# Performance work log

Hardware: AMD Instinct MI355X
Metric: run time of the kernel (lower is better)

## Reference

```python
import jax, jax.numpy as jnp
import numpy as np

# irreps structure: 256x0e + 128x1e + 64x2e (same for all three layers)
MULS = [256, 128, 64]
DIMS = [1, 3, 5]  # 2l+1 for l=0,1,2


def _split(x):
    """Split flat feature [N, 960] into per-irrep blocks [N, mul, 2l+1]."""
    blocks, o = [], 0
    for m, d in zip(MULS, DIMS):
        blocks.append(x[:, o:o + m * d].reshape(-1, m, d))
        o += m * d
    return blocks


def _merge(blocks):
    n = blocks[0].shape[0]
    return jnp.concatenate([b.reshape(n, -1) for b in blocks], axis=1)


def _irrep_linear(blocks, ws):
    # o3.Linear between identical irreps: per-l matmul over the multiplicity
    # axis, path_normalization='element' (single path) -> scale 1/sqrt(mul_in).
    return [jnp.einsum('nui,uw->nwi', b, w) / np.sqrt(b.shape[1])
            for b, w in zip(blocks, ws)]


def _norm_act(blocks):
    # e3nn NormActivation(gelu), normalize=True: x * gelu(||x||) / ||x||
    out = []
    for b in blocks:
        n = jnp.sqrt(jnp.sum(b * b, axis=-1, keepdims=True))  # [N, mul, 1]
        safe_n = jnp.where(n > 0, n, 1.0)
        out.append(b * (jax.nn.gelu(n, approximate=False) / safe_n))
    return out


def setup_inputs() -> dict:
    key = jax.random.key(0)
    ks = jax.random.split(key, 7)
    N = 65536
    D = sum(m * d for m, d in zip(MULS, DIMS))  # 960
    inp = {'x': jax.random.normal(ks[0], (N, D), dtype=jnp.float32)}
    names = ['W0_0', 'W0_1', 'W0_2', 'W1_0', 'W1_1', 'W1_2']
    shapes = [(256, 256), (128, 128), (64, 64)] * 2
    for k, name, s in zip(ks[1:], names, shapes):
        inp[name] = jax.random.normal(k, s, dtype=jnp.float32)
    return inp


def reference(x, W0_0, W0_1, W0_2, W1_0, W1_1, W1_2):
    blocks = _split(x)
    blocks = _irrep_linear(blocks, [W0_0, W0_1, W0_2])
    blocks = _norm_act(blocks)
    blocks = _irrep_linear(blocks, [W1_0, W1_1, W1_2])
    return _merge(blocks)
```

## Files before the change

kernel.cpp:

```cpp
#include <hip/hip_runtime.h>


typedef __bf16 v8bf  __attribute__((ext_vector_type(8)));
typedef float  v4f   __attribute__((ext_vector_type(4)));
typedef unsigned short u16x8 __attribute__((ext_vector_type(8)));

__device__ __forceinline__ unsigned short f2bf(float x) {
    union { float f; unsigned u; } v; v.f = x;
    unsigned r = v.u + 0x7FFFu + ((v.u >> 16) & 1u);
    return (unsigned short)(r >> 16);
}
__device__ __forceinline__ unsigned pk2(float a, float b) {
    return (unsigned)f2bf(a) | ((unsigned)f2bf(b) << 16);
}

__device__ __forceinline__ float phi_from_sq(float s) {
    float n = __builtin_amdgcn_sqrtf(s);
    float z = n * 0.70710678118654752f;
    float t = __builtin_amdgcn_rcpf(fmaf(0.3275911f, z, 1.0f));
    float p = t * fmaf(t, fmaf(t, fmaf(t, fmaf(t, 1.061405429f, -1.453152027f),
                                       1.421413741f), -0.284496736f), 0.254829592f);
    float e = __builtin_amdgcn_exp2f(z * z * -1.4426950408889634f);
    return fmaf(p * e, -0.5f, 1.0f);
}

__global__ __launch_bounds__(256) void wt_prep(
    const float* __restrict__ w0, const float* __restrict__ w1,
    const float* __restrict__ w2, const float* __restrict__ w3,
    const float* __restrict__ w4, const float* __restrict__ w5,
    unsigned short* __restrict__ out)
{
    int t = blockIdx.x * 256 + threadIdx.x;
    if (t >= 172032) return;
    int s = (t < 65536) ? 0 : (t < 81920) ? 1 : (t < 86016) ? 2
          : (t < 151552) ? 3 : (t < 167936) ? 4 : 5;
    int base = (s == 0) ? 0 : (s == 1) ? 65536 : (s == 2) ? 81920
             : (s == 3) ? 86016 : (s == 4) ? 151552 : 167936;
    int lg   = (s == 0 || s == 3) ? 8 : (s == 1 || s == 4) ? 7 : 6;
    float scl = (s == 0 || s == 3) ? 0.0625f
              : (s == 1 || s == 4) ? 0.08838834764831845f : 0.125f;
    const float* p = (s == 0) ? w0 : (s == 1) ? w1 : (s == 2) ? w2
                   : (s == 3) ? w3 : (s == 4) ? w4 : w5;
    int loc = t - base;
    int w = loc >> lg;
    int u = loc & ((1 << lg) - 1);
    out[t] = f2bf(p[(u << lg) + w] * scl);
}

template<int U, int D, int OFF, int ROWS>
__device__ __forceinline__ void irrep_block(
    const float* __restrict__ x,
    const unsigned short* __restrict__ wt0,
    const unsigned short* __restrict__ wt1,
    float* __restrict__ out,
    unsigned short* __restrict__ lds,
    int tile)
{
    constexpr int M    = ROWS * D;
    constexpr int MT   = M / 16;
    constexpr int NPW  = U / 64;
    constexpr int KT   = U / 32;
    constexpr int NR16 = ROWS / 16;

    const int tid  = threadIdx.x;
    const int lane = tid & 63;
    const int wid  = tid >> 6;
    const int row0 = tile * ROWS;

    if constexpr (D == 1) {
        #pragma unroll
        for (int o = 0; o < (ROWS * (U / 8)) / 256; ++o) {
            int oct = o * 256 + tid;
            int row = oct / (U / 8);
            int u0  = (oct % (U / 8)) * 8;
            const float4* p =
                reinterpret_cast<const float4*>(x + (long)(row0 + row) * 960 + OFF + u0);
            float4 fa = p[0], fb = p[1];
            u16x8 hv = { f2bf(fa.x), f2bf(fa.y), f2bf(fa.z), f2bf(fa.w),
                         f2bf(fb.x), f2bf(fb.y), f2bf(fb.z), f2bf(fb.w) };
            int idx = (row * U + u0) ^ ((row & 7) << 3);
            *reinterpret_cast<u16x8*>(&lds[idx]) = hv;
        }
    } else {
        constexpr int PAIRS = U / 2;
        #pragma unroll
        for (int g = 0; g < (ROWS * PAIRS) / 256; ++g) {
            int gid = g * 256 + tid;
            int row = gid / PAIRS;
            int u0  = (gid % PAIRS) * 2;
            const float2* p = reinterpret_cast<const float2*>(
                x + (long)(row0 + row) * 960 + OFF + u0 * D);
            float f[2 * D];
            #pragma unroll
            for (int j = 0; j < D; ++j) { float2 q = p[j]; f[2*j] = q.x; f[2*j+1] = q.y; }
            #pragma unroll
            for (int i = 0; i < D; ++i) {
                int R = i * ROWS + row;
                int idx = (R * U + u0) ^ ((R & 7) << 3);
                *reinterpret_cast<unsigned*>(&lds[idx]) = pk2(f[i], f[D + i]);
            }
        }
    }
    __syncthreads();

    v4f acc[MT][NPW];
    const int kcol = (lane >> 4) << 3;
    const int wcol = lane & 15;
    const int g4   = (lane >> 4) << 2;

    auto run_layer = [&](const unsigned short* __restrict__ wt) {
        #pragma unroll
        for (int mt = 0; mt < MT; ++mt)
            #pragma unroll
            for (int nt = 0; nt < NPW; ++nt) {
                v4f z = {0.f, 0.f, 0.f, 0.f};
                acc[mt][nt] = z;
            }
        #pragma unroll
        for (int kt = 0; kt < KT; ++kt) {
            v8bf b[NPW];
            #pragma unroll
            for (int nt = 0; nt < NPW; ++nt) {
                int w = (wid * NPW + nt) * 16 + wcol;
                b[nt] = *reinterpret_cast<const v8bf*>(wt + w * U + kt * 32 + kcol);
            }
            #pragma unroll
            for (int mt = 0; mt < MT; ++mt) {
                int R = mt * 16 + wcol;
                int idx = (R * U + kt * 32 + kcol) ^ ((R & 7) << 3);
                v8bf a = *reinterpret_cast<const v8bf*>(&lds[idx]);
                #pragma unroll
                for (int nt = 0; nt < NPW; ++nt)
                    acc[mt][nt] = __builtin_amdgcn_mfma_f32_16x16x32_bf16(
                        a, b[nt], acc[mt][nt], 0, 0, 0);
            }
        }
    };

    run_layer(wt0);
    __syncthreads();

    #pragma unroll
    for (int nt = 0; nt < NPW; ++nt) {
        int w = (wid * NPW + nt) * 16 + wcol;
        #pragma unroll
        for (int h = 0; h < NR16; ++h) {
            #pragma unroll
            for (int r = 0; r < 4; ++r) {
                float s = 0.f;
                #pragma unroll
                for (int i = 0; i < D; ++i) {
                    float v = acc[i * NR16 + h][nt][r];
                    s += v * v;
                }
                float fac = phi_from_sq(s);
                int n = h * 16 + g4 + r;
                #pragma unroll
                for (int i = 0; i < D; ++i) {
                    int R = i * ROWS + n;
                    int idx = (R * U + w) ^ ((R & 7) << 3);
                    lds[idx] = f2bf(acc[i * NR16 + h][nt][r] * fac);
                }
            }
        }
    }
    __syncthreads();

    run_layer(wt1);

    #pragma unroll
    for (int nt = 0; nt < NPW; ++nt) {
        int w = (wid * NPW + nt) * 16 + wcol;
        #pragma unroll
        for (int h = 0; h < NR16; ++h) {
            #pragma unroll
            for (int r = 0; r < 4; ++r) {
                int n = row0 + h * 16 + g4 + r;
                float* po = out + (long)n * 960 + OFF + w * D;
                #pragma unroll
                for (int i = 0; i < D; ++i)
                    po[i] = acc[i * NR16 + h][nt][r];
            }
        }
    }
}

__global__ __launch_bounds__(256, 3) void fused_all(
    const float* __restrict__ x,
    const unsigned short* __restrict__ ws,
    float* __restrict__ out)
{
    __shared__ unsigned short lds[16384];
    int bid = blockIdx.x;
    if (bid < 1024)
        irrep_block<256, 1,   0, 64>(x, ws + 0,     ws + 86016,  out, lds, bid);
    else if (bid < 3072)
        irrep_block<128, 3, 256, 32>(x, ws + 65536, ws + 151552, out, lds, bid - 1024);
    else
        irrep_block< 64, 5, 640, 32>(x, ws + 81920, ws + 167936, out, lds, bid - 3072);
}

extern "C" void kernel_launch(void* const* d_in, const int* in_sizes, int n_in,
                              void* d_out, int out_size, void* d_ws, size_t ws_size,
                              hipStream_t stream)
{
    const float* x  = (const float*)d_in[0];
    const float* W0 = (const float*)d_in[1];
    const float* W1 = (const float*)d_in[2];
    const float* W2 = (const float*)d_in[3];
    const float* W3 = (const float*)d_in[4];
    const float* W4 = (const float*)d_in[5];
    const float* W5 = (const float*)d_in[6];
    unsigned short* ws = (unsigned short*)d_ws;
    float* out = (float*)d_out;

    wt_prep<<<672, 256, 0, stream>>>(W0, W1, W2, W3, W4, W5, ws);
    fused_all<<<5120, 256, 0, stream>>>(x, ws, out);
}
```

Baseline: 141.8 us.

## Make fused irrep kernel persistent with double-buffered LDS prefetch of next tile

Replaces the one-tile-per-block launch with a persistent grid of 1024 blocks, each looping over tiles with stride NB. The next tile's input is loaded into registers during the activation and second matmul, then staged into a second LDS buffer, so global loads overlap compute. Tile row counts are halved to fit two 16KB buffers, and the occupancy hint rises to 4 blocks. The cost is extra register pressure from the staged loads, smaller MFMA tiles, and a fixed split of blocks across the three irrep types that may balance work unevenly.

```diff
diff --git a/kernel.cpp b/kernel.cpp
--- a/kernel.cpp
+++ b/kernel.cpp
@@ -3,7 +3,6 @@
 
 typedef __bf16 v8bf  __attribute__((ext_vector_type(8)));
 typedef float  v4f   __attribute__((ext_vector_type(4)));
-typedef unsigned short u16x8 __attribute__((ext_vector_type(8)));
 
 __device__ __forceinline__ unsigned short f2bf(float x) {
     union { float f; unsigned u; } v; v.f = x;
@@ -48,67 +47,101 @@
 }
 
 template<int U, int D, int OFF, int ROWS>
-__device__ __forceinline__ void irrep_block(
+__device__ __forceinline__ void irrep_pipe(
     const float* __restrict__ x,
     const unsigned short* __restrict__ wt0,
     const unsigned short* __restrict__ wt1,
     float* __restrict__ out,
-    unsigned short* __restrict__ lds,
-    int tile)
-{
-    constexpr int M    = ROWS * D;
-    constexpr int MT   = M / 16;
+    unsigned short* lds0, unsigned short* lds1,
+    int t0, int NB)
+{
+    constexpr int NTILES = 65536 / ROWS;
+    constexpr int MT   = (ROWS * D) / 16;
     constexpr int NPW  = U / 64;
     constexpr int KT   = U / 32;
     constexpr int NR16 = ROWS / 16;
+    constexpr int SIT  = (D == 1) ? (ROWS * (U / 8)) / 256
+                                  : (ROWS * (U / 2)) / 256;
 
     const int tid  = threadIdx.x;
     const int lane = tid & 63;
     const int wid  = tid >> 6;
-    const int row0 = tile * ROWS;
-
-    if constexpr (D == 1) {
-        #pragma unroll
-        for (int o = 0; o < (ROWS * (U / 8)) / 256; ++o) {
-            int oct = o * 256 + tid;
-            int row = oct / (U / 8);
-            int u0  = (oct % (U / 8)) * 8;
-            const float4* p =
-                reinterpret_cast<const float4*>(x + (long)(row0 + row) * 960 + OFF + u0);
-            float4 fa = p[0], fb = p[1];
-            u16x8 hv = { f2bf(fa.x), f2bf(fa.y), f2bf(fa.z), f2bf(fa.w),
-                         f2bf(fb.x), f2bf(fb.y), f2bf(fb.z), f2bf(fb.w) };
-            int idx = (row * U + u0) ^ ((row & 7) << 3);
-            *reinterpret_cast<u16x8*>(&lds[idx]) = hv;
-        }
-    } else {
-        constexpr int PAIRS = U / 2;
-        #pragma unroll
-        for (int g = 0; g < (ROWS * PAIRS) / 256; ++g) {
-            int gid = g * 256 + tid;
-            int row = gid / PAIRS;
-            int u0  = (gid % PAIRS) * 2;
-            const float2* p = reinterpret_cast<const float2*>(
-                x + (long)(row0 + row) * 960 + OFF + u0 * D);
-            float f[2 * D];
-            #pragma unroll
-            for (int j = 0; j < D; ++j) { float2 q = p[j]; f[2*j] = q.x; f[2*j+1] = q.y; }
-            #pragma unroll
-            for (int i = 0; i < D; ++i) {
-                int R = i * ROWS + row;
-                int idx = (R * U + u0) ^ ((R & 7) << 3);
-                *reinterpret_cast<unsigned*>(&lds[idx]) = pk2(f[i], f[D + i]);
-            }
-        }
-    }
-    __syncthreads();
+    const int wcol = lane & 15;
+    const int kcol = (lane >> 4) << 3;
+    const int g4   = (lane >> 4) << 2;
+
+    float4 s4[(D == 1) ? SIT * 2 : 1];
+    float2 s2[(D  > 1) ? SIT * D : 1];
+
+    auto issue = [&](int tile) {
+        if constexpr (D == 1) {
+            #pragma unroll
+            for (int o = 0; o < SIT; ++o) {
+                int oct = o * 256 + tid;
+                int row = oct / (U / 8);
+                int u0  = (oct % (U / 8)) * 8;
+                const float4* p = reinterpret_cast<const float4*>(
+                    x + (long)(tile * ROWS + row) * 960 + OFF + u0);
+                s4[o * 2]     = p[0];
+                s4[o * 2 + 1] = p[1];
+            }
+        } else {
+            constexpr int PAIRS = U / 2;
+            #pragma unroll
+            for (int g = 0; g < SIT; ++g) {
+                int gid = g * 256 + tid;
+                int row = gid / PAIRS;
+                int u0  = (gid % PAIRS) * 2;
+                const float2* p = reinterpret_cast<const float2*>(
+                    x + (long)(tile * ROWS + row) * 960 + OFF + u0 * D);
+                #pragma unroll
+                for (int j = 0; j < D; ++j) s2[g * D + j] = p[j];
+            }
+        }
+    };
+
+    auto write_stage = [&](unsigned short* buf) {
+        if constexpr (D == 1) {
+            #pragma unroll
+            for (int o = 0; o < SIT; ++o) {
+                int oct = o * 256 + tid;
+                int row = oct / (U / 8);
+                int u0  = (oct % (U / 8)) * 8;
+                float4 fa = s4[o * 2], fb = s4[o * 2 + 1];
+                uint2 lohi0, lohi1;
+                lohi0.x = pk2(fa.x, fa.y); lohi0.y = pk2(fa.z, fa.w);
+                lohi1.x = pk2(fb.x, fb.y); lohi1.y = pk2(fb.z, fb.w);
+                int idx = (row * U + u0) ^ ((row & 7) << 3);
+                uint4 v; v.x = lohi0.x; v.y = lohi0.y; v.z = lohi1.x; v.w = lohi1.y;
+                *reinterpret_cast<uint4*>(&buf[idx]) = v;
+            }
+        } else {
+            constexpr int PAIRS = U / 2;
+            #pragma unroll
+            for (int g = 0; g < SIT; ++g) {
+                int gid = g * 256 + tid;
+                int row = gid / PAIRS;
+                int u0  = (gid % PAIRS) * 2;
+                float f[2 * D];
+                #pragma unroll
+                for (int j = 0; j < D; ++j) {
+                    float2 q = s2[g * D + j];
+                    f[2 * j] = q.x; f[2 * j + 1] = q.y;
+                }
+                #pragma unroll
+                for (int i = 0; i < D; ++i) {
+                    int R = i * ROWS + row;
+                    int idx = (R * U + u0) ^ ((R & 7) << 3);
+                    *reinterpret_cast<unsigned*>(&buf[idx]) = pk2(f[i], f[D + i]);
+                }
+            }
+        }
+    };
 
     v4f acc[MT][NPW];
-    const int kcol = (lane >> 4) << 3;
-    const int wcol = lane & 15;
-    const int g4   = (lane >> 4) << 2;
-
-    auto run_layer = [&](const unsigned short* __restrict__ wt) {
+
+    auto run_layer = [&](const unsigned short* __restrict__ wt,
+                         const unsigned short* buf) {
         #pragma unroll
         for (int mt = 0; mt < MT; ++mt)
             #pragma unroll
@@ -128,7 +161,7 @@
             for (int mt = 0; mt < MT; ++mt) {
                 int R = mt * 16 + wcol;
                 int idx = (R * U + kt * 32 + kcol) ^ ((R & 7) << 3);
-                v8bf a = *reinterpret_cast<const v8bf*>(&lds[idx]);
+                v8bf a = *reinterpret_cast<const v8bf*>(&buf[idx]);
                 #pragma unroll
                 for (int nt = 0; nt < NPW; ++nt)
                     acc[mt][nt] = __builtin_amdgcn_mfma_f32_16x16x32_bf16(
@@ -137,67 +170,87 @@
         }
     };
 
-    run_layer(wt0);
-    __syncthreads();
-
-    #pragma unroll
-    for (int nt = 0; nt < NPW; ++nt) {
-        int w = (wid * NPW + nt) * 16 + wcol;
-        #pragma unroll
-        for (int h = 0; h < NR16; ++h) {
-            #pragma unroll
-            for (int r = 0; r < 4; ++r) {
-                float s = 0.f;
-                #pragma unroll
-                for (int i = 0; i < D; ++i) {
-                    float v = acc[i * NR16 + h][nt][r];
-                    s += v * v;
-                }
-                float fac = phi_from_sq(s);
-                int n = h * 16 + g4 + r;
-                #pragma unroll
-                for (int i = 0; i < D; ++i) {
-                    int R = i * ROWS + n;
-                    int idx = (R * U + w) ^ ((R & 7) << 3);
-                    lds[idx] = f2bf(acc[i * NR16 + h][nt][r] * fac);
-                }
-            }
-        }
+    int t = t0;
+    issue(t);
+    write_stage(lds0);
+    unsigned short* cur = lds0;
+    unsigned short* nxt = lds1;
+
+    while (t < NTILES) {
+        __syncthreads();
+        run_layer(wt0, cur);
+        __syncthreads();
+
+        int tn = t + NB;
+        issue(tn < NTILES ? tn : t);
+
+        #pragma unroll
+        for (int nt = 0; nt < NPW; ++nt) {
+            int w = (wid * NPW + nt) * 16 + wcol;
+            #pragma unroll
+            for (int h = 0; h < NR16; ++h) {
+                #pragma unroll
+                for (int r = 0; r < 4; ++r) {
+                    float s = 0.f;
+                    #pragma unroll
+                    for (int i = 0; i < D; ++i) {
+                        float v = acc[i * NR16 + h][nt][r];
+                        s += v * v;
+                    }
+                    float fac = phi_from_sq(s);
+                    int n = h * 16 + g4 + r;
+                    #pragma unroll
+                    for (int i = 0; i < D; ++i) {
+                        int R = i * ROWS + n;
+                        int idx = (R * U + w) ^ ((R & 7) << 3);
+                        cur[idx] = f2bf(acc[i * NR16 + h][nt][r] * fac);
+                    }
+                }
+            }
+        }
+        __syncthreads();
+
+        run_layer(wt1, cur);
+
+        write_stage(nxt);
+
+        #pragma unroll
+        for (int nt = 0; nt < NPW; ++nt) {
+            int w = (wid * NPW + nt) * 16 + wcol;
+            #pragma unroll
+            for (int h = 0; h < NR16; ++h) {
+                #pragma unroll
+                for (int r = 0; r < 4; ++r) {
+                    int n = t * ROWS + h * 16 + g4 + r;
+                    float* po = out + (long)n * 960 + OFF + w * D;
+                    #pragma unroll
+                    for (int i = 0; i < D; ++i)
+                        po[i] = acc[i * NR16 + h][nt][r];
+                }
+            }
+        }
+
+        t = tn;
+        unsigned short* tmp = cur; cur = nxt; nxt = tmp;
     }
-    __syncthreads();
-
-    run_layer(wt1);
-
-    #pragma unroll
-    for (int nt = 0; nt < NPW; ++nt) {
-        int w = (wid * NPW + nt) * 16 + wcol;
-        #pragma unroll
-        for (int h = 0; h < NR16; ++h) {
-            #pragma unroll
-            for (int r = 0; r < 4; ++r) {
-                int n = row0 + h * 16 + g4 + r;
-                float* po = out + (long)n * 960 + OFF + w * D;
-                #pragma unroll
-                for (int i = 0; i < D; ++i)
-                    po[i] = acc[i * NR16 + h][nt][r];
-            }
-        }
-    }
-}
-
-__global__ __launch_bounds__(256, 3) void fused_all(
+}
+
+__global__ __launch_bounds__(256, 4) void fused_all(
     const float* __restrict__ x,
     const unsigned short* __restrict__ ws,
     float* __restrict__ out)
 {
-    __shared__ unsigned short lds[16384];
+    __shared__ unsigned short lds[2][8192];
     int bid = blockIdx.x;
-    if (bid < 1024)
-        irrep_block<256, 1,   0, 64>(x, ws + 0,     ws + 86016,  out, lds, bid);
-    else if (bid < 3072)
-        irrep_block<128, 3, 256, 32>(x, ws + 65536, ws + 151552, out, lds, bid - 1024);
+    if (bid < 384)
+        irrep_pipe<256, 1,   0, 32>(x, ws + 0,     ws + 86016,  out,
+                                    lds[0], lds[1], bid, 384);
+    else if (bid < 768)
+        irrep_pipe<128, 3, 256, 16>(x, ws + 65536, ws + 151552, out,
+                                    lds[0], lds[1], bid - 384, 384);
     else
-        irrep_block< 64, 5, 640, 32>(x, ws + 81920, ws + 167936, out, lds, bid - 3072);
+        irrep_pipe< 64, 5, 640, 16>(x, ws + 81920, ws + 167936, out,
+                                    lds[0], lds[1], bid - 768, 256);
 }
 
 extern "C" void kernel_launch(void* const* d_in, const int* in_sizes, int n_in,
@@ -215,5 +268,5 @@
     float* out = (float*)d_out;
 
     wt_prep<<<672, 256, 0, stream>>>(W0, W1, W2, W3, W4, W5, ws);
-    fused_all<<<5120, 256, 0, stream>>>(x, ws, out);
-}
+    fused_all<<<1024, 256, 0, stream>>>(x, ws, out);
+}
```

After: 358.5 us. 2.53x slower.

## Give each wave its own l=0 rows to drop block barriers and LDS staging

Applied to the files above, without the earlier changes.

The l=0 path (256 multiplicity, scalar irreps) gets a dedicated per-wave routine. Each wave owns 16 rows, loads its A operands straight from global memory into registers, and computes all 256 output columns. It stages the gated hidden activations in a private 4096-element LDS slice, so no block-wide __syncthreads are needed. The launch bound minimum is raised from 3 to 4 blocks per CU, which may force register spilling given the 16-accumulator tiles. Each wave now reads the full weight matrix, which raises weight traffic from L2/cache.

```diff
diff --git a/kernel.cpp b/kernel.cpp
--- a/kernel.cpp
+++ b/kernel.cpp
@@ -47,7 +47,94 @@
     out[t] = f2bf(p[(u << lg) + w] * scl);
 }
 
-template<int U, int D, int OFF, int ROWS>
+__device__ __forceinline__ void l0_wave(
+    const float* __restrict__ x,
+    const unsigned short* __restrict__ wt0,
+    const unsigned short* __restrict__ wt1,
+    float* __restrict__ out,
+    unsigned short* hbuf,
+    int tile)
+{
+    const int lane = threadIdx.x & 63;
+    const int wid  = threadIdx.x >> 6;
+    const int l15  = lane & 15;
+    const int oct  = lane >> 4;
+    const int row0 = tile * 64 + wid * 16;
+
+    v4f acc[16];
+    #pragma unroll
+    for (int nt = 0; nt < 16; ++nt) { v4f z = {0.f,0.f,0.f,0.f}; acc[nt] = z; }
+
+    const float* xr = x + (long)(row0 + l15) * 960 + oct * 8;
+    #pragma unroll
+    for (int kt = 0; kt < 8; ++kt) {
+        float4 xa = *reinterpret_cast<const float4*>(xr + kt * 32);
+        float4 xb = *reinterpret_cast<const float4*>(xr + kt * 32 + 4);
+        v8bf a = { (__bf16)xa.x, (__bf16)xa.y, (__bf16)xa.z, (__bf16)xa.w,
+                   (__bf16)xb.x, (__bf16)xb.y, (__bf16)xb.z, (__bf16)xb.w };
+        #pragma unroll
+        for (int hf = 0; hf < 2; ++hf) {
+            v8bf b[8];
+            #pragma unroll
+            for (int j = 0; j < 8; ++j) {
+                int w = (hf * 8 + j) * 16 + l15;
+                b[j] = *reinterpret_cast<const v8bf*>(wt0 + w * 256 + kt * 32 + oct * 8);
+            }
+            #pragma unroll
+            for (int j = 0; j < 8; ++j)
+                acc[hf * 8 + j] = __builtin_amdgcn_mfma_f32_16x16x32_bf16(
+                    a, b[j], acc[hf * 8 + j], 0, 0, 0);
+        }
+    }
+
+    #pragma unroll
+    for (int nt = 0; nt < 16; ++nt) {
+        int w = nt * 16 + l15;
+        #pragma unroll
+        for (int r = 0; r < 4; ++r) {
+            float h   = acc[nt][r];
+            float fac = phi_from_sq(h * h);
+            int R   = oct * 4 + r;
+            int idx = (R * 256 + w) ^ ((R & 7) << 3);
+            hbuf[idx] = f2bf(h * fac);
+        }
+    }
+    asm volatile("s_waitcnt lgkmcnt(0)" ::: "memory");
+    __builtin_amdgcn_sched_barrier(0);
+
+    #pragma unroll
+    for (int nt = 0; nt < 16; ++nt) { v4f z = {0.f,0.f,0.f,0.f}; acc[nt] = z; }
+    #pragma unroll
+    for (int kt = 0; kt < 8; ++kt) {
+        int idx = (l15 * 256 + kt * 32 + oct * 8) ^ ((l15 & 7) << 3);
+        v8bf a = *reinterpret_cast<const v8bf*>(&hbuf[idx]);
+        #pragma unroll
+        for (int hf = 0; hf < 2; ++hf) {
+            v8bf b[8];
+            #pragma unroll
+            for (int j = 0; j < 8; ++j) {
+                int w = (hf * 8 + j) * 16 + l15;
+                b[j] = *reinterpret_cast<const v8bf*>(wt1 + w * 256 + kt * 32 + oct * 8);
+            }
+            #pragma unroll
+            for (int j = 0; j < 8; ++j)
+                acc[hf * 8 + j] = __builtin_amdgcn_mfma_f32_16x16x32_bf16(
+                    a, b[j], acc[hf * 8 + j], 0, 0, 0);
+        }
+    }
+
+    #pragma unroll
+    for (int nt = 0; nt < 16; ++nt) {
+        int w = nt * 16 + l15;
+        #pragma unroll
+        for (int r = 0; r < 4; ++r) {
+            int n = row0 + oct * 4 + r;
+            out[(long)n * 960 + w] = acc[nt][r];
+        }
+    }
+}
+
+template<int U, int D, int OFF>
 __device__ __forceinline__ void irrep_block(
     const float* __restrict__ x,
     const unsigned short* __restrict__ wt0,
@@ -56,8 +143,8 @@
     unsigned short* __restrict__ lds,
     int tile)
 {
-    constexpr int M    = ROWS * D;
-    constexpr int MT   = M / 16;
+    constexpr int ROWS = 32;
+    constexpr int MT   = (ROWS * D) / 16;
     constexpr int NPW  = U / 64;
     constexpr int KT   = U / 32;
     constexpr int NR16 = ROWS / 16;
@@ -67,38 +154,22 @@
     const int wid  = tid >> 6;
     const int row0 = tile * ROWS;
 
-    if constexpr (D == 1) {
-        #pragma unroll
-        for (int o = 0; o < (ROWS * (U / 8)) / 256; ++o) {
-            int oct = o * 256 + tid;
-            int row = oct / (U / 8);
-            int u0  = (oct % (U / 8)) * 8;
-            const float4* p =
-                reinterpret_cast<const float4*>(x + (long)(row0 + row) * 960 + OFF + u0);
-            float4 fa = p[0], fb = p[1];
-            u16x8 hv = { f2bf(fa.x), f2bf(fa.y), f2bf(fa.z), f2bf(fa.w),
-                         f2bf(fb.x), f2bf(fb.y), f2bf(fb.z), f2bf(fb.w) };
-            int idx = (row * U + u0) ^ ((row & 7) << 3);
-            *reinterpret_cast<u16x8*>(&lds[idx]) = hv;
-        }
-    } else {
-        constexpr int PAIRS = U / 2;
-        #pragma unroll
-        for (int g = 0; g < (ROWS * PAIRS) / 256; ++g) {
-            int gid = g * 256 + tid;
-            int row = gid / PAIRS;
-            int u0  = (gid % PAIRS) * 2;
-            const float2* p = reinterpret_cast<const float2*>(
-                x + (long)(row0 + row) * 960 + OFF + u0 * D);
-            float f[2 * D];
-            #pragma unroll
-            for (int j = 0; j < D; ++j) { float2 q = p[j]; f[2*j] = q.x; f[2*j+1] = q.y; }
-            #pragma unroll
-            for (int i = 0; i < D; ++i) {
-                int R = i * ROWS + row;
-                int idx = (R * U + u0) ^ ((R & 7) << 3);
-                *reinterpret_cast<unsigned*>(&lds[idx]) = pk2(f[i], f[D + i]);
-            }
+    constexpr int PAIRS = U / 2;
+    #pragma unroll
+    for (int g = 0; g < (ROWS * PAIRS) / 256; ++g) {
+        int gid = g * 256 + tid;
+        int row = gid / PAIRS;
+        int u0  = (gid % PAIRS) * 2;
+        const float2* p = reinterpret_cast<const float2*>(
+            x + (long)(row0 + row) * 960 + OFF + u0 * D);
+        float f[2 * D];
+        #pragma unroll
+        for (int j = 0; j < D; ++j) { float2 q = p[j]; f[2*j] = q.x; f[2*j+1] = q.y; }
+        #pragma unroll
+        for (int i = 0; i < D; ++i) {
+            int R = i * ROWS + row;
+            int idx = (R * U + u0) ^ ((R & 7) << 3);
+            *reinterpret_cast<unsigned*>(&lds[idx]) = pk2(f[i], f[D + i]);
         }
     }
     __syncthreads();
@@ -185,7 +256,7 @@
     }
 }
 
-__global__ __launch_bounds__(256, 3) void fused_all(
+__global__ __launch_bounds__(256, 4) void fused_all(
     const float* __restrict__ x,
     const unsigned short* __restrict__ ws,
     float* __restrict__ out)
@@ -193,11 +264,12 @@
     __shared__ unsigned short lds[16384];
     int bid = blockIdx.x;
     if (bid < 1024)
-        irrep_block<256, 1,   0, 64>(x, ws + 0,     ws + 86016,  out, lds, bid);
+        l0_wave(x, ws + 0, ws + 86016, out,
+                lds + (threadIdx.x >> 6) * 4096, bid);
     else if (bid < 3072)
-        irrep_block<128, 3, 256, 32>(x, ws + 65536, ws + 151552, out, lds, bid - 1024);
+        irrep_block<128, 3, 256>(x, ws + 65536, ws + 151552, out, lds, bid - 1024);
     else
-        irrep_block< 64, 5, 640, 32>(x, ws + 81920, ws + 167936, out, lds, bid - 3072);
+        irrep_block< 64, 5, 640>(x, ws + 81920, ws + 167936, out, lds, bid - 3072);
 }
 
 extern "C" void kernel_launch(void* const* d_in, const int* in_sizes, int n_in,
```

New measurement: 250.3 us. 1.77x slower.

## Prefetch weight fragments one k-step ahead and raise occupancy target

Applied to the files above, without the earlier changes.

The kernel now loads the B (weight) fragments for the next k-tile while MFMAs on the current tile run, and issues the first fragment load of each layer before the preceding barrier. For l=0 it uses fabs instead of sqrt(x*x) in the norm. The launch bound moves from 3 to 4 blocks per CU, which adds register pressure and risks spills because of the extra prefetch registers.

```diff
diff --git a/kernel.cpp b/kernel.cpp
--- a/kernel.cpp
+++ b/kernel.cpp
@@ -14,8 +14,7 @@
     return (unsigned)f2bf(a) | ((unsigned)f2bf(b) << 16);
 }
 
-__device__ __forceinline__ float phi_from_sq(float s) {
-    float n = __builtin_amdgcn_sqrtf(s);
+__device__ __forceinline__ float phi_from_n(float n) {
     float z = n * 0.70710678118654752f;
     float t = __builtin_amdgcn_rcpf(fmaf(0.3275911f, z, 1.0f));
     float p = t * fmaf(t, fmaf(t, fmaf(t, fmaf(t, 1.061405429f, -1.453152027f),
@@ -56,16 +55,19 @@
     unsigned short* __restrict__ lds,
     int tile)
 {
-    constexpr int M    = ROWS * D;
-    constexpr int MT   = M / 16;
+    constexpr int MT   = (ROWS * D) / 16;
     constexpr int NPW  = U / 64;
     constexpr int KT   = U / 32;
     constexpr int NR16 = ROWS / 16;
+    static_assert(ROWS * D * U <= 16384, "LDS overflow");
 
     const int tid  = threadIdx.x;
     const int lane = tid & 63;
     const int wid  = tid >> 6;
     const int row0 = tile * ROWS;
+    const int wcol = lane & 15;
+    const int kcol = (lane >> 4) << 3;
+    const int g4   = (lane >> 4) << 2;
 
     if constexpr (D == 1) {
         #pragma unroll
@@ -101,12 +103,17 @@
             }
         }
     }
-    __syncthreads();
 
     v4f acc[MT][NPW];
-    const int kcol = (lane >> 4) << 3;
-    const int wcol = lane & 15;
-    const int g4   = (lane >> 4) << 2;
+    v8bf bpre[NPW];
+
+    auto issueB = [&](const unsigned short* __restrict__ wt, int kt) {
+        #pragma unroll
+        for (int nt = 0; nt < NPW; ++nt) {
+            int w = (wid * NPW + nt) * 16 + wcol;
+            bpre[nt] = *reinterpret_cast<const v8bf*>(wt + w * U + kt * 32 + kcol);
+        }
+    };
 
     auto run_layer = [&](const unsigned short* __restrict__ wt) {
         #pragma unroll
@@ -118,12 +125,10 @@
             }
         #pragma unroll
         for (int kt = 0; kt < KT; ++kt) {
-            v8bf b[NPW];
-            #pragma unroll
-            for (int nt = 0; nt < NPW; ++nt) {
-                int w = (wid * NPW + nt) * 16 + wcol;
-                b[nt] = *reinterpret_cast<const v8bf*>(wt + w * U + kt * 32 + kcol);
-            }
+            v8bf bcur[NPW];
+            #pragma unroll
+            for (int nt = 0; nt < NPW; ++nt) bcur[nt] = bpre[nt];
+            if (kt + 1 < KT) issueB(wt, kt + 1);
             #pragma unroll
             for (int mt = 0; mt < MT; ++mt) {
                 int R = mt * 16 + wcol;
@@ -132,13 +137,18 @@
                 #pragma unroll
                 for (int nt = 0; nt < NPW; ++nt)
                     acc[mt][nt] = __builtin_amdgcn_mfma_f32_16x16x32_bf16(
-                        a, b[nt], acc[mt][nt], 0, 0, 0);
+                        a, bcur[nt], acc[mt][nt], 0, 0, 0);
             }
         }
     };
+
+    issueB(wt0, 0);
+    __syncthreads();
 
     run_layer(wt0);
     __syncthreads();
+
+    issueB(wt1, 0);
 
     #pragma unroll
     for (int nt = 0; nt < NPW; ++nt) {
@@ -147,17 +157,23 @@
         for (int h = 0; h < NR16; ++h) {
             #pragma unroll
             for (int r = 0; r < 4; ++r) {
-                float s = 0.f;
+                float n;
+                if constexpr (D == 1) {
+                    n = __builtin_fabsf(acc[h][nt][r]);
+                } else {
+                    float s = 0.f;
+                    #pragma unroll
+                    for (int i = 0; i < D; ++i) {
+                        float v = acc[i * NR16 + h][nt][r];
+                        s += v * v;
+                    }
+                    n = __builtin_amdgcn_sqrtf(s);
+                }
+                float fac = phi_from_n(n);
+                int nr = h * 16 + g4 + r;
                 #pragma unroll
                 for (int i = 0; i < D; ++i) {
-                    float v = acc[i * NR16 + h][nt][r];
-                    s += v * v;
-                }
-                float fac = phi_from_sq(s);
-                int n = h * 16 + g4 + r;
-                #pragma unroll
-                for (int i = 0; i < D; ++i) {
-                    int R = i * ROWS + n;
+                    int R = i * ROWS + nr;
                     int idx = (R * U + w) ^ ((R & 7) << 3);
                     lds[idx] = f2bf(acc[i * NR16 + h][nt][r] * fac);
                 }
@@ -185,7 +201,7 @@
     }
 }
 
-__global__ __launch_bounds__(256, 3) void fused_all(
+__global__ __launch_bounds__(256, 4) void fused_all(
     const float* __restrict__ x,
     const unsigned short* __restrict__ ws,
     float* __restrict__ out)
```

Result: no change. 141.7 us (-0.1%).
